# Optimization experiments

Measured on AMD Instinct MI355X. Metric: run time of the kernel, lower is better.

## Reference

```python
import jax, jax.numpy as jnp
import numpy as np

STRIDE = 4
HEADS = 8
KSIZE = 5
PAD_L = 4  # causal: kernel_size - 1


def _layernorm(x, g, b, eps=1e-5):
    mu = jnp.mean(x, axis=-1, keepdims=True)
    var = jnp.mean((x - mu) ** 2, axis=-1, keepdims=True)
    return (x - mu) * jax.lax.rsqrt(var + eps) * g + b


def setup_inputs() -> dict:
    key = jax.random.key(0)
    ks = jax.random.split(key, 6)
    B, T, C = 8, 2048, 1024
    D = 4096
    x = jax.random.normal(ks[0], (B, T, C), dtype=jnp.float32)
    W_proj = jax.random.normal(ks[1], (C * STRIDE, D), dtype=jnp.float32) * 0.02
    b_proj = jnp.zeros((D,), dtype=jnp.float32)
    ln_g = jnp.ones((D,), dtype=jnp.float32)
    ln_b = jnp.zeros((D,), dtype=jnp.float32)
    W_wgen = jax.random.normal(ks[2], (D, HEADS * KSIZE), dtype=jnp.float32) * 0.02
    b_wgen = jnp.zeros((HEADS * KSIZE,), dtype=jnp.float32)
    W_ff = jax.random.normal(ks[3], (D, D), dtype=jnp.float32) * 0.02
    b_ff = jnp.zeros((D,), dtype=jnp.float32)
    return {"x": x, "W_proj": W_proj, "b_proj": b_proj, "ln_g": ln_g, "ln_b": ln_b,
            "W_wgen": W_wgen, "b_wgen": b_wgen, "W_ff": W_ff, "b_ff": b_ff}


def reference(x, W_proj, b_proj, ln_g, ln_b, W_wgen, b_wgen, W_ff, b_ff):
    B, T, C = x.shape
    folded_T = T // STRIDE
    # fold time into channels, then dense projection to llm_dim
    xf = x[:, : folded_T * STRIDE].reshape(B, folded_T, C * STRIDE)
    h = xf @ W_proj + b_proj  # [B, Tf, D]
    D = h.shape[-1]
    R = D // HEADS
    # LConv1DBlock with norm_before + dynamic conv + (linear, relu, dropout p=0) + residual
    res = h
    y = _layernorm(h, ln_g, ln_b)
    # per-position dynamic weights, softmax over kernel taps
    w = (y @ W_wgen + b_wgen).reshape(B, folded_T, HEADS, KSIZE)
    w = jax.nn.softmax(w, axis=-1)  # [B, Tf, H, K]
    # causal depthwise conv: out[t] = sum_k w[t,k] * y[t - (K-1) + k]
    yp = jnp.pad(y, ((0, 0), (PAD_L, 0), (0, 0)))  # left pad time
    # stacked taps: [K, B, Tf, H, R]
    taps = jnp.stack([yp[:, k:k + folded_T] for k in range(KSIZE)], axis=0)
    taps = taps.reshape(KSIZE, B, folded_T, HEADS, R)
    conv = jnp.einsum('kbthr,bthk->bthr', taps, w).reshape(B, folded_T, D)
    # feed-forward ops: linear -> relu -> dropout(p=0)
    out = res + jax.nn.relu(conv @ W_ff + b_ff)
    return out
```

## Files before the change

kernel.cpp:

```cpp
#include <hip/hip_runtime.h>

typedef unsigned short u16;
typedef unsigned int u32;
typedef __attribute__((ext_vector_type(8))) short bf16x8;
typedef __attribute__((ext_vector_type(4))) float f32x4;

__device__ __forceinline__ float bf2f(u16 u) {
    union { u32 i; float f; } x; x.i = ((u32)u) << 16; return x.f;
}
__device__ __forceinline__ u16 f2bf(float f) {
    union { float f; u32 i; } x; x.f = f;
    u32 u = x.i;
    u += 0x7FFFu + ((u >> 16) & 1u);
    return (u16)(u >> 16);
}
__device__ __forceinline__ float wred(float v) {
    #pragma unroll
    for (int off = 32; off; off >>= 1) v += __shfl_down(v, off);
    return v;
}
__device__ __forceinline__ void gload_lds16(const void* g, void* l) {
    __builtin_amdgcn_global_load_lds(
        (const __attribute__((address_space(1))) u32*)g,
        (__attribute__((address_space(3))) u32*)l,
        16, 0, 0);
}

__global__ __launch_bounds__(256)
void cvt_f32_bf16(const float* __restrict__ in, u16* __restrict__ out) {
    int i = (blockIdx.x * 256 + threadIdx.x) * 4;
    float4 v = *(const float4*)(in + i);
    ushort4 p;
    p.x = f2bf(v.x); p.y = f2bf(v.y); p.z = f2bf(v.z); p.w = f2bf(v.w);
    *(ushort4*)(out + i) = p;
}

__global__ __launch_bounds__(256)
void transpose_cvt(const float* __restrict__ W, u16* __restrict__ Wt) {
    __shared__ float tile[64][65];
    int n0 = blockIdx.x * 64;
    int k0 = blockIdx.y * 64;
    int tx = threadIdx.x, ty = threadIdx.y;
    #pragma unroll
    for (int i = 0; i < 8; ++i) {
        int kk = ty + i * 8;
        const float* src = W + (size_t)(k0 + kk) * 4096 + n0;
        tile[kk][tx]      = src[tx];
        tile[kk][tx + 32] = src[tx + 32];
    }
    __syncthreads();
    #pragma unroll
    for (int i = 0; i < 8; ++i) {
        int nn = ty + i * 8;
        ushort2 p;
        p.x = f2bf(tile[tx * 2][nn]);
        p.y = f2bf(tile[tx * 2 + 1][nn]);
        *(ushort2*)(Wt + (size_t)(n0 + nn) * 4096 + k0 + tx * 2) = p;
    }
}

__global__ __launch_bounds__(256)
void transpose_wgen(const float* __restrict__ W, float* __restrict__ Wt) {
    int idx = blockIdx.x * 256 + threadIdx.x;
    int c = idx >> 12, e = idx & 4095;
    Wt[idx] = W[(size_t)e * 40 + c];
}

template <int MODE>
__global__ __launch_bounds__(512, 2)
void gemm256(const u16* __restrict__ A, const u16* __restrict__ Bt,
             const float* __restrict__ bias, const float* __restrict__ res,
             float* __restrict__ out) {
    const int K = 4096, N = 4096;
    __shared__ u16 smem[65536];

    const int tid = threadIdx.x;
    const int lane = tid & 63;
    const int w = tid >> 6;
    const int wr = w >> 2, wc = w & 3;
    const int fr = lane & 15;
    const int fk = (lane >> 4) * 8;
    const int cswz = (fr & 7) << 3;

    const int bid = blockIdx.x;
    const int swz = (bid & 7) * (gridDim.x >> 3) + (bid >> 3);
    const int tm = swz >> 4, tn = swz & 15;
    const size_t rowA0 = (size_t)tm * 256;
    const size_t rowB0 = (size_t)tn * 256;

    const int srl = lane >> 3;
    const int scl = ((lane & 7) ^ srl) << 3;

    f32x4 acc[8][4] = {};
    bf16x8 af[8];
    bf16x8 bh0[4];
    bf16x8 bh1[4];

    auto stA = [&](int b, int half, int kt) {
        #pragma unroll
        for (int i = 0; i < 2; ++i) {
            size_t grow = rowA0 + half * 128 + i * 64 + w * 8 + srl;
            gload_lds16(A + grow * K + kt * 64 + scl,
                        &smem[b * 32768 + half * 8192 + i * 4096 + w * 512 + lane * 8]);
        }
    };
    auto stB = [&](int b, int half, int kt) {
        #pragma unroll
        for (int i = 0; i < 2; ++i) {
            size_t grow = rowB0 + half * 128 + i * 64 + w * 8 + srl;
            gload_lds16(Bt + grow * K + kt * 64 + scl,
                        &smem[b * 32768 + 16384 + half * 8192 + i * 4096 + w * 512 + lane * 8]);
        }
    };
    auto ldA = [&](int b, int qm) {
        #pragma unroll
        for (int m = 0; m < 4; ++m) {
            int base = b * 32768 + (wr * 128 + (qm * 4 + m) * 16 + fr) * 64;
            af[m * 2 + 0] = *(const bf16x8*)&smem[base + (fk ^ cswz)];
            af[m * 2 + 1] = *(const bf16x8*)&smem[base + ((32 + fk) ^ cswz)];
        }
    };
    auto ldB = [&](int b, int qn, bf16x8 (&bh)[4]) {
        #pragma unroll
        for (int n = 0; n < 2; ++n) {
            int base = b * 32768 + 16384 + (wc * 64 + qn * 32 + n * 16 + fr) * 64;
            bh[n * 2 + 0] = *(const bf16x8*)&smem[base + (fk ^ cswz)];
            bh[n * 2 + 1] = *(const bf16x8*)&smem[base + ((32 + fk) ^ cswz)];
        }
    };
    auto mma = [&](int qm, int qn, bf16x8 (&bh)[4]) {
        __builtin_amdgcn_s_setprio(1);
        #pragma unroll
        for (int m = 0; m < 4; ++m)
            #pragma unroll
            for (int n = 0; n < 2; ++n) {
                acc[qm*4+m][qn*2+n] = __builtin_amdgcn_mfma_f32_16x16x32_bf16(
                    af[m*2+0], bh[n*2+0], acc[qm*4+m][qn*2+n], 0, 0, 0);
                acc[qm*4+m][qn*2+n] = __builtin_amdgcn_mfma_f32_16x16x32_bf16(
                    af[m*2+1], bh[n*2+1], acc[qm*4+m][qn*2+n], 0, 0, 0);
            }
        __builtin_amdgcn_s_setprio(0);
    };
    #define BAR() __builtin_amdgcn_s_barrier()
    #define VM4() asm volatile("s_waitcnt vmcnt(4)" ::: "memory")

    stB(0, 0, 0); stB(0, 1, 0); stA(0, 0, 0); stA(0, 1, 0);
    stB(1, 0, 1); stB(1, 1, 1);
    VM4();
    BAR();

    for (int i = 0; i < 32; ++i) {
        const int t = 2 * i;
        const int kt2 = (t + 2 < 64) ? t + 2 : 63;
        const int kt3 = (t + 3 < 64) ? t + 3 : 63;
        ldA(0, 0); ldB(0, 0, bh0);
        stA(1, 0, t + 1);
        BAR(); mma(0, 0, bh0);
        ldB(0, 1, bh1);
        stA(1, 1, t + 1);
        BAR(); mma(0, 1, bh1);
        ldA(0, 1);
        BAR(); mma(1, 1, bh1);
        stB(0, 0, kt2); stB(0, 1, kt2);
        VM4();
        BAR(); mma(1, 0, bh0);
        ldA(1, 0); ldB(1, 0, bh0);
        stA(0, 0, kt2);
        BAR(); mma(0, 0, bh0);
        ldB(1, 1, bh1);
        stA(0, 1, kt2);
        BAR(); mma(0, 1, bh1);
        ldA(1, 1);
        BAR(); mma(1, 1, bh1);
        stB(1, 0, kt3); stB(1, 1, kt3);
        VM4();
        BAR(); mma(1, 0, bh0);
    }
    #undef BAR
    #undef VM4

    const int cc = lane & 15;
    const int cr = (lane >> 4) * 4;
    #pragma unroll
    for (int m = 0; m < 8; ++m) {
        #pragma unroll
        for (int n = 0; n < 4; ++n) {
            size_t row = rowA0 + wr * 128 + m * 16 + cr;
            size_t col = rowB0 + wc * 64 + n * 16 + cc;
            float bv = bias[col];
            #pragma unroll
            for (int q = 0; q < 4; ++q) {
                size_t idx = (row + q) * (size_t)N + col;
                float v = acc[m][n][q] + bv;
                if (MODE == 1) v = res[idx] + fmaxf(v, 0.0f);
                out[idx] = v;
            }
        }
    }
}

__global__ __launch_bounds__(256)
void ln_wgen(const float* __restrict__ h, const float* __restrict__ g,
             const float* __restrict__ beta, const float* __restrict__ WgT,
             const float* __restrict__ bg, u16* __restrict__ y,
             float* __restrict__ w) {
    __shared__ u32 ylp[8][2048];
    __shared__ float red[8];
    __shared__ float wraw[8][40];

    int tid = threadIdx.x, lane = tid & 63, wv = tid >> 6;
    size_t row0 = (size_t)blockIdx.x * 8;

    for (int r = 0; r < 8; ++r) {
        const float4* hr = (const float4*)(h + (row0 + r) * 4096);
        float4 v[4];
        float s = 0.f, ss = 0.f;
        #pragma unroll
        for (int i = 0; i < 4; ++i) {
            v[i] = hr[tid + i * 256];
            s  += v[i].x + v[i].y + v[i].z + v[i].w;
            ss += v[i].x * v[i].x + v[i].y * v[i].y + v[i].z * v[i].z + v[i].w * v[i].w;
        }
        s = wred(s); ss = wred(ss);
        if (lane == 0) { red[wv] = s; red[4 + wv] = ss; }
        __syncthreads();
        float S = red[0] + red[1] + red[2] + red[3];
        float SS = red[4] + red[5] + red[6] + red[7];
        float mu = S * (1.0f / 4096.0f);
        float var = SS * (1.0f / 4096.0f) - mu * mu;
        float inv = rsqrtf(var + 1e-5f);
        u16* yr = y + (row0 + r) * 4096;
        #pragma unroll
        for (int i = 0; i < 4; ++i) {
            int base = tid + i * 256;
            float4 gv = ((const float4*)g)[base];
            float4 bv = ((const float4*)beta)[base];
            float o0 = (v[i].x - mu) * inv * gv.x + bv.x;
            float o1 = (v[i].y - mu) * inv * gv.y + bv.y;
            float o2 = (v[i].z - mu) * inv * gv.z + bv.z;
            float o3 = (v[i].w - mu) * inv * gv.w + bv.w;
            u32 p01 = (u32)f2bf(o0) | ((u32)f2bf(o1) << 16);
            u32 p23 = (u32)f2bf(o2) | ((u32)f2bf(o3) << 16);
            ylp[r][base * 2]     = p01;
            ylp[r][base * 2 + 1] = p23;
            uint2 pk; pk.x = p01; pk.y = p23;
            *(uint2*)(yr + base * 4) = pk;
        }
        __syncthreads();
    }

    float acc[8][10];
    #pragma unroll
    for (int r = 0; r < 8; ++r)
        #pragma unroll
        for (int c = 0; c < 10; ++c) acc[r][c] = 0.f;

    for (int eb = lane; eb < 2048; eb += 64) {
        float alo[8], ahi[8];
        #pragma unroll
        for (int r = 0; r < 8; ++r) {
            u32 a = ylp[r][eb];
            alo[r] = bf2f((u16)a);
            ahi[r] = bf2f((u16)(a >> 16));
        }
        #pragma unroll
        for (int c0 = 0; c0 < 10; ++c0) {
            int c = wv * 10 + c0;
            float2 wg = ((const float2*)(WgT + (size_t)c * 4096))[eb];
            #pragma unroll
            for (int r = 0; r < 8; ++r)
                acc[r][c0] += alo[r] * wg.x + ahi[r] * wg.y;
        }
    }
    #pragma unroll
    for (int r = 0; r < 8; ++r) {
        #pragma unroll
        for (int c0 = 0; c0 < 10; ++c0) {
            float p = wred(acc[r][c0]);
            if (lane == 0) wraw[r][wv * 10 + c0] = p + bg[wv * 10 + c0];
        }
    }
    __syncthreads();

    if (tid < 64) {
        int r = tid >> 3, hh = tid & 7;
        float e5[5];
        float mx = -1e30f;
        #pragma unroll
        for (int k = 0; k < 5; ++k) mx = fmaxf(mx, wraw[r][hh * 5 + k]);
        float sum = 0.f;
        #pragma unroll
        for (int k = 0; k < 5; ++k) { e5[k] = expf(wraw[r][hh * 5 + k] - mx); sum += e5[k]; }
        float isum = 1.0f / sum;
        float* wp = w + (row0 + r) * 40 + hh * 5;
        #pragma unroll
        for (int k = 0; k < 5; ++k) wp[k] = e5[k] * isum;
    }
}

__global__ __launch_bounds__(256)
void dconv2(const u16* __restrict__ y, const float* __restrict__ w,
            u16* __restrict__ conv) {
    int bid = blockIdx.x;
    int half = bid & 1;
    int rem = bid >> 1;
    int tc = rem % 18, b = rem / 18;
    int t0 = tc * 30;
    int d0 = half * 2048 + threadIdx.x * 8;
    int head = d0 >> 9;
    const u16* yb = y + (size_t)b * 512 * 4096 + d0;
    u16* cb = conv + (size_t)b * 512 * 4096 + d0;
    const float* wb = w + ((size_t)b * 512) * 40 + head * 5;

    float ring[5][8];
    #pragma unroll
    for (int j = 0; j < 4; ++j) {
        int tt = t0 - 4 + j;
        if (tt >= 0) {
            uint4 v = *(const uint4*)(yb + (size_t)tt * 4096);
            const u16* us = (const u16*)&v;
            #pragma unroll
            for (int e = 0; e < 8; ++e) ring[j + 1][e] = bf2f(us[e]);
        } else {
            #pragma unroll
            for (int e = 0; e < 8; ++e) ring[j + 1][e] = 0.f;
        }
    }

    for (int tt = 0; tt < 30; tt += 5) {
        #pragma unroll
        for (int j = 0; j < 5; ++j) {
            int t = t0 + tt + j;
            if (t < 512) {
                uint4 v = *(const uint4*)(yb + (size_t)t * 4096);
                const u16* us = (const u16*)&v;
                #pragma unroll
                for (int e = 0; e < 8; ++e) ring[j][e] = bf2f(us[e]);
                const float* wt = wb + (size_t)t * 40;
                float w0 = wt[0], w1 = wt[1], w2 = wt[2], w3 = wt[3], w4 = wt[4];
                u16 o[8];
                #pragma unroll
                for (int e = 0; e < 8; ++e) {
                    float a = w0 * ring[(j + 1) % 5][e]
                            + w1 * ring[(j + 2) % 5][e]
                            + w2 * ring[(j + 3) % 5][e]
                            + w3 * ring[(j + 4) % 5][e]
                            + w4 * ring[j][e];
                    o[e] = f2bf(a);
                }
                *(uint4*)(cb + (size_t)t * 4096) = *(uint4*)o;
            }
        }
    }
}

extern "C" void kernel_launch(void* const* d_in, const int* in_sizes, int n_in,
                              void* d_out, int out_size, void* d_ws, size_t ws_size,
                              hipStream_t stream) {
    const float* x      = (const float*)d_in[0];
    const float* W_proj = (const float*)d_in[1];
    const float* b_proj = (const float*)d_in[2];
    const float* ln_g   = (const float*)d_in[3];
    const float* ln_b   = (const float*)d_in[4];
    const float* W_wgen = (const float*)d_in[5];
    const float* b_wgen = (const float*)d_in[6];
    const float* W_ff   = (const float*)d_in[7];
    const float* b_ff   = (const float*)d_in[8];
    float* out = (float*)d_out;

    char* ws = (char*)d_ws;
    u16* xb   = (u16*)(ws);
    u16* WpT  = (u16*)(ws + ((size_t)32 << 20));
    u16* WfT  = (u16*)(ws + ((size_t)64 << 20));
    float* wbuf = (float*)(ws + ((size_t)96 << 20));
    float* WgT  = (float*)(ws + ((size_t)97 << 20));
    u16* conv = xb;
    u16* ybuf = WpT;

    cvt_f32_bf16<<<16384, 256, 0, stream>>>(x, xb);
    dim3 tb(32, 8);
    transpose_cvt<<<dim3(64, 64), tb, 0, stream>>>(W_proj, WpT);
    transpose_cvt<<<dim3(64, 64), tb, 0, stream>>>(W_ff, WfT);
    transpose_wgen<<<640, 256, 0, stream>>>(W_wgen, WgT);

    gemm256<0><<<256, 512, 0, stream>>>(xb, WpT, b_proj, nullptr, out);
    ln_wgen<<<512, 256, 0, stream>>>(out, ln_g, ln_b, WgT, b_wgen, ybuf, wbuf);
    dconv2<<<288, 256, 0, stream>>>(ybuf, wbuf, conv);
    gemm256<1><<<256, 512, 0, stream>>>(conv, WfT, b_ff, out, out);
}
```

Before: 359.2 us.

## Switch GEMM to 32x32x16 MFMA tiles and retile dynamic conv kernel

The 256x256 GEMM now uses 32x32x16 bf16 MFMA instructions instead of 16x16x32, which changes the LDS fragment loads, the accumulator layout and the epilogue indexing. The larger MFMA shape needs fewer LDS reads per flop and fewer instructions. The depthwise conv kernel is also rewritten with a fully unrolled 16-step shift-register window and 512 blocks instead of 288, to improve occupancy and remove the modulo ring indexing. The cost is more halo reloads per block in the conv and different register pressure in the GEMM.

```diff
diff --git a/kernel.cpp b/kernel.cpp
--- a/kernel.cpp
+++ b/kernel.cpp
@@ -4,6 +4,7 @@
 typedef unsigned int u32;
 typedef __attribute__((ext_vector_type(8))) short bf16x8;
 typedef __attribute__((ext_vector_type(4))) float f32x4;
+typedef __attribute__((ext_vector_type(16))) float f32x16;
 
 __device__ __forceinline__ float bf2f(u16 u) {
     union { u32 i; float f; } x; x.i = ((u32)u) << 16; return x.f;
@@ -78,9 +79,9 @@
     const int lane = tid & 63;
     const int w = tid >> 6;
     const int wr = w >> 2, wc = w & 3;
-    const int fr = lane & 15;
-    const int fk = (lane >> 4) * 8;
-    const int cswz = (fr & 7) << 3;
+    const int l31 = lane & 31;
+    const int hi = lane >> 5;
+    const int l7 = lane & 7;
 
     const int bid = blockIdx.x;
     const int swz = (bid & 7) * (gridDim.x >> 3) + (bid >> 3);
@@ -91,7 +92,7 @@
     const int srl = lane >> 3;
     const int scl = ((lane & 7) ^ srl) << 3;
 
-    f32x4 acc[8][4] = {};
+    f32x16 acc[4][2] = {};
     bf16x8 af[8];
     bf16x8 bh0[4];
     bf16x8 bh1[4];
@@ -114,31 +115,29 @@
     };
     auto ldA = [&](int b, int qm) {
         #pragma unroll
-        for (int m = 0; m < 4; ++m) {
-            int base = b * 32768 + (wr * 128 + (qm * 4 + m) * 16 + fr) * 64;
-            af[m * 2 + 0] = *(const bf16x8*)&smem[base + (fk ^ cswz)];
-            af[m * 2 + 1] = *(const bf16x8*)&smem[base + ((32 + fk) ^ cswz)];
+        for (int mt = 0; mt < 2; ++mt) {
+            int row = wr * 128 + qm * 64 + mt * 32 + l31;
+            int base = b * 32768 + row * 64;
+            #pragma unroll
+            for (int kk = 0; kk < 4; ++kk)
+                af[mt * 4 + kk] = *(const bf16x8*)&smem[base + (((kk * 2 + hi) ^ l7) << 3)];
         }
     };
     auto ldB = [&](int b, int qn, bf16x8 (&bh)[4]) {
-        #pragma unroll
-        for (int n = 0; n < 2; ++n) {
-            int base = b * 32768 + 16384 + (wc * 64 + qn * 32 + n * 16 + fr) * 64;
-            bh[n * 2 + 0] = *(const bf16x8*)&smem[base + (fk ^ cswz)];
-            bh[n * 2 + 1] = *(const bf16x8*)&smem[base + ((32 + fk) ^ cswz)];
-        }
+        int row = wc * 64 + qn * 32 + l31;
+        int base = b * 32768 + 16384 + row * 64;
+        #pragma unroll
+        for (int kk = 0; kk < 4; ++kk)
+            bh[kk] = *(const bf16x8*)&smem[base + (((kk * 2 + hi) ^ l7) << 3)];
     };
     auto mma = [&](int qm, int qn, bf16x8 (&bh)[4]) {
         __builtin_amdgcn_s_setprio(1);
         #pragma unroll
-        for (int m = 0; m < 4; ++m)
+        for (int kk = 0; kk < 4; ++kk)
             #pragma unroll
-            for (int n = 0; n < 2; ++n) {
-                acc[qm*4+m][qn*2+n] = __builtin_amdgcn_mfma_f32_16x16x32_bf16(
-                    af[m*2+0], bh[n*2+0], acc[qm*4+m][qn*2+n], 0, 0, 0);
-                acc[qm*4+m][qn*2+n] = __builtin_amdgcn_mfma_f32_16x16x32_bf16(
-                    af[m*2+1], bh[n*2+1], acc[qm*4+m][qn*2+n], 0, 0, 0);
-            }
+            for (int mt = 0; mt < 2; ++mt)
+                acc[qm * 2 + mt][qn] = __builtin_amdgcn_mfma_f32_32x32x16_bf16(
+                    af[mt * 4 + kk], bh[kk], acc[qm * 2 + mt][qn], 0, 0, 0);
         __builtin_amdgcn_s_setprio(0);
     };
     #define BAR() __builtin_amdgcn_s_barrier()
@@ -179,21 +178,22 @@
     #undef BAR
     #undef VM4
 
-    const int cc = lane & 15;
-    const int cr = (lane >> 4) * 4;
-    #pragma unroll
-    for (int m = 0; m < 8; ++m) {
-        #pragma unroll
-        for (int n = 0; n < 4; ++n) {
-            size_t row = rowA0 + wr * 128 + m * 16 + cr;
-            size_t col = rowB0 + wc * 64 + n * 16 + cc;
+    #pragma unroll
+    for (int mt = 0; mt < 4; ++mt) {
+        #pragma unroll
+        for (int nt = 0; nt < 2; ++nt) {
+            size_t rowb = rowA0 + wr * 128 + mt * 32 + hi * 4;
+            size_t col = rowB0 + wc * 64 + nt * 32 + l31;
             float bv = bias[col];
             #pragma unroll
-            for (int q = 0; q < 4; ++q) {
-                size_t idx = (row + q) * (size_t)N + col;
-                float v = acc[m][n][q] + bv;
-                if (MODE == 1) v = res[idx] + fmaxf(v, 0.0f);
-                out[idx] = v;
+            for (int g = 0; g < 4; ++g) {
+                #pragma unroll
+                for (int q = 0; q < 4; ++q) {
+                    size_t idx = (rowb + 8 * g + q) * (size_t)N + col;
+                    float v = acc[mt][nt][g * 4 + q] + bv;
+                    if (MODE == 1) v = res[idx] + fmaxf(v, 0.0f);
+                    out[idx] = v;
+                }
             }
         }
     }
@@ -299,58 +299,57 @@
 }
 
 __global__ __launch_bounds__(256)
-void dconv2(const u16* __restrict__ y, const float* __restrict__ w,
+void dconv3(const u16* __restrict__ y, const float* __restrict__ w,
             u16* __restrict__ conv) {
     int bid = blockIdx.x;
     int half = bid & 1;
     int rem = bid >> 1;
-    int tc = rem % 18, b = rem / 18;
-    int t0 = tc * 30;
+    int tc = rem & 31, b = rem >> 5;
+    int t0 = tc * 16;
     int d0 = half * 2048 + threadIdx.x * 8;
     int head = d0 >> 9;
     const u16* yb = y + (size_t)b * 512 * 4096 + d0;
     u16* cb = conv + (size_t)b * 512 * 4096 + d0;
     const float* wb = w + ((size_t)b * 512) * 40 + head * 5;
 
-    float ring[5][8];
-    #pragma unroll
-    for (int j = 0; j < 4; ++j) {
-        int tt = t0 - 4 + j;
-        if (tt >= 0) {
-            uint4 v = *(const uint4*)(yb + (size_t)tt * 4096);
-            const u16* us = (const u16*)&v;
-            #pragma unroll
-            for (int e = 0; e < 8; ++e) ring[j + 1][e] = bf2f(us[e]);
-        } else {
-            #pragma unroll
-            for (int e = 0; e < 8; ++e) ring[j + 1][e] = 0.f;
-        }
-    }
-
-    for (int tt = 0; tt < 30; tt += 5) {
-        #pragma unroll
-        for (int j = 0; j < 5; ++j) {
-            int t = t0 + tt + j;
-            if (t < 512) {
-                uint4 v = *(const uint4*)(yb + (size_t)t * 4096);
+    float r0[8], r1[8], r2[8], r3[8], r4[8];
+    {
+        float* slots[4] = { r1, r2, r3, r4 };
+        #pragma unroll
+        for (int j = 0; j < 4; ++j) {
+            int tt = t0 - 4 + j;
+            if (tt >= 0) {
+                uint4 v = *(const uint4*)(yb + (size_t)tt * 4096);
                 const u16* us = (const u16*)&v;
                 #pragma unroll
-                for (int e = 0; e < 8; ++e) ring[j][e] = bf2f(us[e]);
-                const float* wt = wb + (size_t)t * 40;
-                float w0 = wt[0], w1 = wt[1], w2 = wt[2], w3 = wt[3], w4 = wt[4];
-                u16 o[8];
+                for (int e = 0; e < 8; ++e) slots[j][e] = bf2f(us[e]);
+            } else {
                 #pragma unroll
-                for (int e = 0; e < 8; ++e) {
-                    float a = w0 * ring[(j + 1) % 5][e]
-                            + w1 * ring[(j + 2) % 5][e]
-                            + w2 * ring[(j + 3) % 5][e]
-                            + w3 * ring[(j + 4) % 5][e]
-                            + w4 * ring[j][e];
-                    o[e] = f2bf(a);
-                }
-                *(uint4*)(cb + (size_t)t * 4096) = *(uint4*)o;
+                for (int e = 0; e < 8; ++e) slots[j][e] = 0.f;
             }
         }
+    }
+
+    #pragma unroll
+    for (int tt = 0; tt < 16; ++tt) {
+        int t = t0 + tt;
+        #pragma unroll
+        for (int e = 0; e < 8; ++e) {
+            r0[e] = r1[e]; r1[e] = r2[e]; r2[e] = r3[e]; r3[e] = r4[e];
+        }
+        uint4 v = *(const uint4*)(yb + (size_t)t * 4096);
+        const u16* us = (const u16*)&v;
+        #pragma unroll
+        for (int e = 0; e < 8; ++e) r4[e] = bf2f(us[e]);
+        const float* wt = wb + (size_t)t * 40;
+        float w0 = wt[0], w1 = wt[1], w2 = wt[2], w3 = wt[3], w4 = wt[4];
+        u16 o[8];
+        #pragma unroll
+        for (int e = 0; e < 8; ++e) {
+            float a = w0 * r0[e] + w1 * r1[e] + w2 * r2[e] + w3 * r3[e] + w4 * r4[e];
+            o[e] = f2bf(a);
+        }
+        *(uint4*)(cb + (size_t)t * 4096) = *(uint4*)o;
     }
 }
 
@@ -385,6 +384,6 @@
 
     gemm256<0><<<256, 512, 0, stream>>>(xb, WpT, b_proj, nullptr, out);
     ln_wgen<<<512, 256, 0, stream>>>(out, ln_g, ln_b, WgT, b_wgen, ybuf, wbuf);
-    dconv2<<<288, 256, 0, stream>>>(ybuf, wbuf, conv);
+    dconv3<<<512, 256, 0, stream>>>(ybuf, wbuf, conv);
     gemm256<1><<<256, 512, 0, stream>>>(conv, WfT, b_ff, out, out);
 }
```

Result: slower. 389.5 us (+8.4%).
